# Kernel tuning notes

Hardware: AMD Instinct MI355X
Metric: run time of the kernel (lower is better)

## Reference

```python
import jax, jax.numpy as jnp
import numpy as np

B, F, E, H, L = 64, 512, 256, 8, 4  # batch, feature_dim(seq), embed_dim, heads, layers
D = E // H                          # head dim = 32


def setup_inputs() -> dict:
    key = jax.random.key(0)
    ks = jax.random.split(key, 12)
    def w(k, shape, fan_in):
        return jax.random.normal(k, shape, jnp.float32) / np.sqrt(fan_in)
    return {
        "features": jax.random.normal(ks[0], (B, F), jnp.float32),
        "emb_w": w(ks[1], (1, E), 1), "emb_b": w(ks[2], (E,), 1),
        "q_w": w(ks[3], (E, E), E), "q_b": w(ks[4], (E,), E),
        "k_w": w(ks[5], (E, E), E), "k_b": w(ks[6], (E,), E),
        "v_w": w(ks[7], (E, E), E), "v_b": w(ks[8], (E,), E),
        "attn_w": w(ks[9], (E, 1), E), "attn_b": w(ks[10], (1,), E),
    }


def reference(features, emb_w, emb_b, q_w, q_b, k_w, k_b, v_w, v_b, attn_w, attn_b):
    # features: [B, F] -> per-feature scalar embedded to E dims
    emb = features[..., None] @ emb_w + emb_b          # [B, F, E]
    # Q path: input is zeros -> embedding gives emb_b, then query linear; constant per position
    q_vec = emb_b @ q_w + q_b                          # [E]
    Q = jnp.broadcast_to(q_vec, (B, F, E)).reshape(B, F, H, D).transpose(0, 2, 1, 3)  # [B,H,F,D]
    K = (emb @ k_w + k_b).reshape(B, F, H, D).transpose(0, 2, 1, 3)
    V = (emb @ v_w + v_b).reshape(B, F, H, D).transpose(0, 2, 1, 3)
    scale = 1.0 / np.sqrt(D)
    v_sum = V.sum(axis=2, keepdims=True)               # [B,H,1,D]; ones@V row-sums
    Qc = Qnc = Q
    for _ in range(L):
        A = jax.nn.softmax(jnp.einsum('bhfd,bhgd->bhfg', Q, K) * scale, axis=-1)
        Qc = jnp.einsum('bhfg,bhgd->bhfd', A, V)       # A @ V
        Qnc = v_sum - Qc                                # (1 - A) @ V, identical math
        Q = Qc
    def merge(t):
        return t.transpose(0, 2, 1, 3).reshape(B, F, E)
    h_ox = (merge(Qc) @ attn_w + attn_b)[..., 0]       # [B, F]
    h_c = (merge(Qnc) @ attn_w + attn_b)[..., 0]       # [B, F]
    return (h_ox, h_c)
```

## Files before the change

kernel.cpp:

```cpp
#include <hip/hip_runtime.h>

#define BB 64
#define FF 512
#define EE 256
#define HH 8
#define DD 32
#define LL 4

__global__ __launch_bounds__(256) void tm_fused_kernel(
    const float* __restrict__ x,
    const float* __restrict__ emb_w,
    const float* __restrict__ emb_b,
    const float* __restrict__ q_w,
    const float* __restrict__ q_b,
    const float* __restrict__ k_w,
    const float* __restrict__ k_b,
    const float* __restrict__ v_w,
    const float* __restrict__ v_b,
    const float* __restrict__ attn_w,
    const float* __restrict__ attn_b,
    float* __restrict__ out)
{
    const int tid = threadIdx.x;
    const int b = blockIdx.x;
    const int g = tid >> 6;
    const int c = (tid & 63) << 2;

    __shared__ float s_ew[EE], s_eb[EE];
    __shared__ float s_red[5][4 * EE];
    __shared__ float s_a0[HH], s_c1[HH], s_c2[HH], s_p1[HH], s_p0[HH], s_m[HH];
    __shared__ float s_hox, s_hc;

    s_ew[tid] = emb_w[tid];
    s_eb[tid] = emb_b[tid];
    __syncthreads();

    float4 kw4 = {0,0,0,0}, kb4 = {0,0,0,0}, vw4 = {0,0,0,0},
           vb4 = {0,0,0,0}, qv4 = {0,0,0,0};
    #pragma unroll 4
    for (int j4 = 0; j4 < 64; ++j4) {
        const int j = (j4 << 2) + g;
        const float ew = s_ew[j], eb = s_eb[j];
        const float4 K = *(const float4*)(k_w + j * EE + c);
        const float4 V = *(const float4*)(v_w + j * EE + c);
        const float4 Q = *(const float4*)(q_w + j * EE + c);
        kw4.x = fmaf(ew, K.x, kw4.x); kw4.y = fmaf(ew, K.y, kw4.y);
        kw4.z = fmaf(ew, K.z, kw4.z); kw4.w = fmaf(ew, K.w, kw4.w);
        kb4.x = fmaf(eb, K.x, kb4.x); kb4.y = fmaf(eb, K.y, kb4.y);
        kb4.z = fmaf(eb, K.z, kb4.z); kb4.w = fmaf(eb, K.w, kb4.w);
        vw4.x = fmaf(ew, V.x, vw4.x); vw4.y = fmaf(ew, V.y, vw4.y);
        vw4.z = fmaf(ew, V.z, vw4.z); vw4.w = fmaf(ew, V.w, vw4.w);
        vb4.x = fmaf(eb, V.x, vb4.x); vb4.y = fmaf(eb, V.y, vb4.y);
        vb4.z = fmaf(eb, V.z, vb4.z); vb4.w = fmaf(eb, V.w, vb4.w);
        qv4.x = fmaf(eb, Q.x, qv4.x); qv4.y = fmaf(eb, Q.y, qv4.y);
        qv4.z = fmaf(eb, Q.z, qv4.z); qv4.w = fmaf(eb, Q.w, qv4.w);
    }
    const int ri = (g << 8) + c;
    *(float4*)&s_red[0][ri] = kw4;
    *(float4*)&s_red[1][ri] = kb4;
    *(float4*)&s_red[2][ri] = vw4;
    *(float4*)&s_red[3][ri] = vb4;
    *(float4*)&s_red[4][ri] = qv4;
    __syncthreads();

    float kw = s_red[0][tid] + s_red[0][256 + tid] + s_red[0][512 + tid] + s_red[0][768 + tid];
    float kb = s_red[1][tid] + s_red[1][256 + tid] + s_red[1][512 + tid] + s_red[1][768 + tid];
    float vw = s_red[2][tid] + s_red[2][256 + tid] + s_red[2][512 + tid] + s_red[2][768 + tid];
    float vb = s_red[3][tid] + s_red[3][256 + tid] + s_red[3][512 + tid] + s_red[3][768 + tid];
    float qv = s_red[4][tid] + s_red[4][256 + tid] + s_red[4][512 + tid] + s_red[4][768 + tid];
    kb += k_b[tid];
    vb += v_b[tid];
    qv += q_b[tid];
    const float aw = attn_w[tid];

    const float scale = 0.17677669529663687f;

    float t0 = qv * kw;
    float t1 = vw * kw;
    float t2 = vb * kw;
    float t3 = vw * aw;
    float t4 = vb * aw;
    for (int off = 16; off > 0; off >>= 1) {
        t0 += __shfl_xor(t0, off, 32);
        t1 += __shfl_xor(t1, off, 32);
        t2 += __shfl_xor(t2, off, 32);
        t3 += __shfl_xor(t3, off, 32);
        t4 += __shfl_xor(t4, off, 32);
    }
    if ((tid & 31) == 0) {
        const int h = tid >> 5;
        s_a0[h] = t0 * scale;
        s_c1[h] = t1;
        s_c2[h] = t2;
        s_p1[h] = t3;
        s_p0[h] = t4;
    }
    __syncthreads();

    const int h = tid >> 5;
    const int lane = tid & 31;

    float xr[16];
    #pragma unroll
    for (int k = 0; k < 4; ++k) {
        const float4 xv = *(const float4*)(x + b * FF + (lane << 2) + (k << 7));
        xr[4 * k + 0] = xv.x; xr[4 * k + 1] = xv.y;
        xr[4 * k + 2] = xv.z; xr[4 * k + 3] = xv.w;
    }

    float sx = 0.f;
    #pragma unroll
    for (int k = 0; k < 16; ++k) sx += xr[k];
    for (int off = 16; off > 0; off >>= 1) sx += __shfl_xor(sx, off, 32);

    float a = s_a0[h];
    const float c1 = s_c1[h], c2 = s_c2[h];
    float m = 0.f;
    for (int it = 0; it < LL; ++it) {
        float p[16];
        float mx = -3.4e38f;
        #pragma unroll
        for (int k = 0; k < 16; ++k) {
            p[k] = a * xr[k];
            mx = fmaxf(mx, p[k]);
        }
        for (int off = 16; off > 0; off >>= 1) mx = fmaxf(mx, __shfl_xor(mx, off, 32));
        float s0 = 0.f, s1 = 0.f;
        #pragma unroll
        for (int k = 0; k < 16; ++k) {
            const float e = __expf(p[k] - mx);
            s0 += e;
            s1 = fmaf(e, xr[k], s1);
        }
        for (int off = 16; off > 0; off >>= 1) {
            s0 += __shfl_xor(s0, off, 32);
            s1 += __shfl_xor(s1, off, 32);
        }
        m = s1 / s0;
        a = scale * fmaf(m, c1, c2);
    }
    if (lane == 0) s_m[h] = m;
    __syncthreads();

    if (tid == 0) {
        const float ab = attn_b[0];
        float hox = ab, hc = ab;
        for (int hh = 0; hh < HH; ++hh) {
            const float qc = fmaf(s_m[hh], s_p1[hh], s_p0[hh]);
            hox += qc;
            hc += fmaf(sx, s_p1[hh], (float)FF * s_p0[hh]) - qc;
        }
        s_hox = hox;
        s_hc = hc;
    }
    __syncthreads();

    const float hox = s_hox, hc = s_hc;
    out[b * FF + tid]                 = hox;
    out[b * FF + tid + 256]           = hox;
    out[BB * FF + b * FF + tid]       = hc;
    out[BB * FF + b * FF + tid + 256] = hc;
}

extern "C" void kernel_launch(void* const* d_in, const int* in_sizes, int n_in,
                              void* d_out, int out_size, void* d_ws, size_t ws_size,
                              hipStream_t stream) {
    const float* features = (const float*)d_in[0];
    const float* emb_w    = (const float*)d_in[1];
    const float* emb_b    = (const float*)d_in[2];
    const float* q_w      = (const float*)d_in[3];
    const float* q_b      = (const float*)d_in[4];
    const float* k_w      = (const float*)d_in[5];
    const float* k_b      = (const float*)d_in[6];
    const float* v_w      = (const float*)d_in[7];
    const float* v_b      = (const float*)d_in[8];
    const float* attn_w   = (const float*)d_in[9];
    const float* attn_b   = (const float*)d_in[10];
    float* out = (float*)d_out;

    tm_fused_kernel<<<dim3(BB), dim3(256), 0, stream>>>(
        features, emb_w, emb_b, q_w, q_b, k_w, k_b, v_w, v_b, attn_w, attn_b, out);
}
```

Baseline: 86.77 us.

## Widen block to 1024 threads to split weight-folding reduction across 16 groups

The block grows from 256 to 1024 threads so the per-block reduction over the three 256x256 weight matrices is split into 16 row groups instead of 4. Each thread's serial loop shrinks from 64 to 16 rows, and the final shared-memory sum reads 16 partials. The unused k_b accumulator is dropped, since the softmax is invariant to it, and the feature loads are issued before the first barrier. In exchange, shared memory and barrier cost grow, only 256 threads stay active in the softmax phase, and every block still re-reads all of the weights.

```diff
diff --git a/kernel.cpp b/kernel.cpp
--- a/kernel.cpp
+++ b/kernel.cpp
@@ -6,8 +6,9 @@
 #define HH 8
 #define DD 32
 #define LL 4
+#define NG 16
 
-__global__ __launch_bounds__(256) void tm_fused_kernel(
+__global__ __launch_bounds__(1024) void tm_fused_kernel(
     const float* __restrict__ x,
     const float* __restrict__ emb_w,
     const float* __restrict__ emb_b,
@@ -25,29 +26,39 @@
     const int b = blockIdx.x;
     const int g = tid >> 6;
     const int c = (tid & 63) << 2;
+    const float scale = 0.17677669529663687f;
 
     __shared__ float s_ew[EE], s_eb[EE];
-    __shared__ float s_red[5][4 * EE];
+    __shared__ float s_red[4][NG * EE];
     __shared__ float s_a0[HH], s_c1[HH], s_c2[HH], s_p1[HH], s_p0[HH], s_m[HH];
     __shared__ float s_hox, s_hc;
 
-    s_ew[tid] = emb_w[tid];
-    s_eb[tid] = emb_b[tid];
+    float xr[16];
+    float aw = 0.f;
+    if (tid < 256) {
+        const int lane = tid & 31;
+        #pragma unroll
+        for (int k = 0; k < 4; ++k) {
+            const float4 xv = *(const float4*)(x + b * FF + (lane << 2) + (k << 7));
+            xr[4 * k + 0] = xv.x; xr[4 * k + 1] = xv.y;
+            xr[4 * k + 2] = xv.z; xr[4 * k + 3] = xv.w;
+        }
+        aw = attn_w[tid];
+        s_ew[tid] = emb_w[tid];
+        s_eb[tid] = emb_b[tid];
+    }
     __syncthreads();
 
-    float4 kw4 = {0,0,0,0}, kb4 = {0,0,0,0}, vw4 = {0,0,0,0},
-           vb4 = {0,0,0,0}, qv4 = {0,0,0,0};
+    float4 kw4 = {0,0,0,0}, vw4 = {0,0,0,0}, vb4 = {0,0,0,0}, qv4 = {0,0,0,0};
     #pragma unroll 4
-    for (int j4 = 0; j4 < 64; ++j4) {
-        const int j = (j4 << 2) + g;
+    for (int j4 = 0; j4 < NG; ++j4) {
+        const int j = (j4 << 4) + g;
         const float ew = s_ew[j], eb = s_eb[j];
         const float4 K = *(const float4*)(k_w + j * EE + c);
         const float4 V = *(const float4*)(v_w + j * EE + c);
         const float4 Q = *(const float4*)(q_w + j * EE + c);
         kw4.x = fmaf(ew, K.x, kw4.x); kw4.y = fmaf(ew, K.y, kw4.y);
         kw4.z = fmaf(ew, K.z, kw4.z); kw4.w = fmaf(ew, K.w, kw4.w);
-        kb4.x = fmaf(eb, K.x, kb4.x); kb4.y = fmaf(eb, K.y, kb4.y);
-        kb4.z = fmaf(eb, K.z, kb4.z); kb4.w = fmaf(eb, K.w, kb4.w);
         vw4.x = fmaf(ew, V.x, vw4.x); vw4.y = fmaf(ew, V.y, vw4.y);
         vw4.z = fmaf(ew, V.z, vw4.z); vw4.w = fmaf(ew, V.w, vw4.w);
         vb4.x = fmaf(eb, V.x, vb4.x); vb4.y = fmaf(eb, V.y, vb4.y);
@@ -55,111 +66,103 @@
         qv4.x = fmaf(eb, Q.x, qv4.x); qv4.y = fmaf(eb, Q.y, qv4.y);
         qv4.z = fmaf(eb, Q.z, qv4.z); qv4.w = fmaf(eb, Q.w, qv4.w);
     }
-    const int ri = (g << 8) + c;
+    const int ri = g * EE + c;
     *(float4*)&s_red[0][ri] = kw4;
-    *(float4*)&s_red[1][ri] = kb4;
-    *(float4*)&s_red[2][ri] = vw4;
-    *(float4*)&s_red[3][ri] = vb4;
-    *(float4*)&s_red[4][ri] = qv4;
+    *(float4*)&s_red[1][ri] = vw4;
+    *(float4*)&s_red[2][ri] = vb4;
+    *(float4*)&s_red[3][ri] = qv4;
     __syncthreads();
 
-    float kw = s_red[0][tid] + s_red[0][256 + tid] + s_red[0][512 + tid] + s_red[0][768 + tid];
-    float kb = s_red[1][tid] + s_red[1][256 + tid] + s_red[1][512 + tid] + s_red[1][768 + tid];
-    float vw = s_red[2][tid] + s_red[2][256 + tid] + s_red[2][512 + tid] + s_red[2][768 + tid];
-    float vb = s_red[3][tid] + s_red[3][256 + tid] + s_red[3][512 + tid] + s_red[3][768 + tid];
-    float qv = s_red[4][tid] + s_red[4][256 + tid] + s_red[4][512 + tid] + s_red[4][768 + tid];
-    kb += k_b[tid];
-    vb += v_b[tid];
-    qv += q_b[tid];
-    const float aw = attn_w[tid];
+    if (tid < 256) {
+        float kw = 0.f, vw = 0.f, vb = 0.f, qv = 0.f;
+        #pragma unroll
+        for (int gg = 0; gg < NG; ++gg) {
+            kw += s_red[0][gg * EE + tid];
+            vw += s_red[1][gg * EE + tid];
+            vb += s_red[2][gg * EE + tid];
+            qv += s_red[3][gg * EE + tid];
+        }
+        vb += v_b[tid];
+        qv += q_b[tid];
 
-    const float scale = 0.17677669529663687f;
-
-    float t0 = qv * kw;
-    float t1 = vw * kw;
-    float t2 = vb * kw;
-    float t3 = vw * aw;
-    float t4 = vb * aw;
-    for (int off = 16; off > 0; off >>= 1) {
-        t0 += __shfl_xor(t0, off, 32);
-        t1 += __shfl_xor(t1, off, 32);
-        t2 += __shfl_xor(t2, off, 32);
-        t3 += __shfl_xor(t3, off, 32);
-        t4 += __shfl_xor(t4, off, 32);
-    }
-    if ((tid & 31) == 0) {
-        const int h = tid >> 5;
-        s_a0[h] = t0 * scale;
-        s_c1[h] = t1;
-        s_c2[h] = t2;
-        s_p1[h] = t3;
-        s_p0[h] = t4;
+        float t0 = qv * kw;
+        float t1 = vw * kw;
+        float t2 = vb * kw;
+        float t3 = vw * aw;
+        float t4 = vb * aw;
+        for (int off = 16; off > 0; off >>= 1) {
+            t0 += __shfl_xor(t0, off, 32);
+            t1 += __shfl_xor(t1, off, 32);
+            t2 += __shfl_xor(t2, off, 32);
+            t3 += __shfl_xor(t3, off, 32);
+            t4 += __shfl_xor(t4, off, 32);
+        }
+        if ((tid & 31) == 0) {
+            const int h = tid >> 5;
+            s_a0[h] = t0 * scale;
+            s_c1[h] = t1;
+            s_c2[h] = t2;
+            s_p1[h] = t3;
+            s_p0[h] = t4;
+        }
     }
     __syncthreads();
 
-    const int h = tid >> 5;
-    const int lane = tid & 31;
+    float sx = 0.f;
+    if (tid < 256) {
+        const int h = tid >> 5;
+        const int lane = tid & 31;
 
-    float xr[16];
-    #pragma unroll
-    for (int k = 0; k < 4; ++k) {
-        const float4 xv = *(const float4*)(x + b * FF + (lane << 2) + (k << 7));
-        xr[4 * k + 0] = xv.x; xr[4 * k + 1] = xv.y;
-        xr[4 * k + 2] = xv.z; xr[4 * k + 3] = xv.w;
+        #pragma unroll
+        for (int k = 0; k < 16; ++k) sx += xr[k];
+        for (int off = 16; off > 0; off >>= 1) sx += __shfl_xor(sx, off, 32);
+
+        float a = s_a0[h];
+        const float c1 = s_c1[h], c2 = s_c2[h];
+        float m = 0.f;
+        for (int it = 0; it < LL; ++it) {
+            float mx = -3.4e38f;
+            #pragma unroll
+            for (int k = 0; k < 16; ++k) mx = fmaxf(mx, a * xr[k]);
+            for (int off = 16; off > 0; off >>= 1) mx = fmaxf(mx, __shfl_xor(mx, off, 32));
+            float s0 = 0.f, s1 = 0.f;
+            #pragma unroll
+            for (int k = 0; k < 16; ++k) {
+                const float e = __expf(fmaf(a, xr[k], -mx));
+                s0 += e;
+                s1 = fmaf(e, xr[k], s1);
+            }
+            for (int off = 16; off > 0; off >>= 1) {
+                s0 += __shfl_xor(s0, off, 32);
+                s1 += __shfl_xor(s1, off, 32);
+            }
+            m = s1 / s0;
+            a = scale * fmaf(m, c1, c2);
+        }
+        if (lane == 0) s_m[h] = m;
+        if (tid == 0) s_hox = sx;
     }
-
-    float sx = 0.f;
-    #pragma unroll
-    for (int k = 0; k < 16; ++k) sx += xr[k];
-    for (int off = 16; off > 0; off >>= 1) sx += __shfl_xor(sx, off, 32);
-
-    float a = s_a0[h];
-    const float c1 = s_c1[h], c2 = s_c2[h];
-    float m = 0.f;
-    for (int it = 0; it < LL; ++it) {
-        float p[16];
-        float mx = -3.4e38f;
-        #pragma unroll
-        for (int k = 0; k < 16; ++k) {
-            p[k] = a * xr[k];
-            mx = fmaxf(mx, p[k]);
-        }
-        for (int off = 16; off > 0; off >>= 1) mx = fmaxf(mx, __shfl_xor(mx, off, 32));
-        float s0 = 0.f, s1 = 0.f;
-        #pragma unroll
-        for (int k = 0; k < 16; ++k) {
-            const float e = __expf(p[k] - mx);
-            s0 += e;
-            s1 = fmaf(e, xr[k], s1);
-        }
-        for (int off = 16; off > 0; off >>= 1) {
-            s0 += __shfl_xor(s0, off, 32);
-            s1 += __shfl_xor(s1, off, 32);
-        }
-        m = s1 / s0;
-        a = scale * fmaf(m, c1, c2);
-    }
-    if (lane == 0) s_m[h] = m;
     __syncthreads();
 
     if (tid == 0) {
         const float ab = attn_b[0];
+        const float sxv = s_hox;
         float hox = ab, hc = ab;
         for (int hh = 0; hh < HH; ++hh) {
             const float qc = fmaf(s_m[hh], s_p1[hh], s_p0[hh]);
             hox += qc;
-            hc += fmaf(sx, s_p1[hh], (float)FF * s_p0[hh]) - qc;
+            hc += fmaf(sxv, s_p1[hh], (float)FF * s_p0[hh]) - qc;
         }
         s_hox = hox;
         s_hc = hc;
     }
     __syncthreads();
 
-    const float hox = s_hox, hc = s_hc;
-    out[b * FF + tid]                 = hox;
-    out[b * FF + tid + 256]           = hox;
-    out[BB * FF + b * FF + tid]       = hc;
-    out[BB * FF + b * FF + tid + 256] = hc;
+    if (tid < FF) {
+        out[b * FF + tid] = s_hox;
+    } else {
+        out[BB * FF + b * FF + (tid - FF)] = s_hc;
+    }
 }
 
 extern "C" void kernel_launch(void* const* d_in, const int* in_sizes, int n_in,
@@ -178,6 +181,6 @@
     const float* attn_b   = (const float*)d_in[10];
     float* out = (float*)d_out;
 
-    tm_fused_kernel<<<dim3(BB), dim3(256), 0, stream>>>(
+    tm_fused_kernel<<<dim3(BB), dim3(1024), 0, stream>>>(
         features, emb_w, emb_b, q_w, q_b, k_w, k_b, v_w, v_b, attn_w, attn_b, out);
 }
```

Result: faster. 83.54 us (-3.7%).
